# Optimization experiments

Hardware: AMD Instinct MI355X
Metric: run time of the kernel (lower is better)

Reference implementation:

```python
import jax, jax.numpy as jnp
import numpy as np

ALPHA = 2.0  # spikingjelly default ATan surrogate alpha
EPS = 1e-5   # BatchNorm eps

@jax.custom_vjp
def heaviside_atan(x):
    return (x >= 0.0).astype(x.dtype)

def _ha_fwd(x):
    return heaviside_atan(x), x

def _ha_bwd(x, g):
    return (g * ALPHA / (2.0 * (1.0 + (jnp.pi / 2.0 * ALPHA * x) ** 2)),)

heaviside_atan.defvjp(_ha_fwd, _ha_bwd)

def lif(x_seq, tau=2.0, v_th=1.0):
    # MultiStepLIFNode, v_reset=0 (hard reset), detach_reset=True
    def step(v, x):
        v = v + (x - v) / tau
        s = heaviside_atan(v - v_th)
        v = v * (1.0 - jax.lax.stop_gradient(s))
        return v, s
    _, spikes = jax.lax.scan(step, jnp.zeros_like(x_seq[0]), x_seq)
    return spikes

def conv_bn(y, Wt, g, b):
    # 1x1 conv (no bias) + BatchNorm2d in training mode over flattened (T*B, H, W)
    y = jnp.einsum('tbchw,oc->tbohw', y, Wt)
    m = y.mean(axis=(0, 1, 3, 4), keepdims=True)
    v = y.var(axis=(0, 1, 3, 4), keepdims=True)
    C = Wt.shape[0]
    return (y - m) / jnp.sqrt(v + EPS) * g.reshape(1, 1, C, 1, 1) + b.reshape(1, 1, C, 1, 1)

def setup_inputs() -> dict:
    key = jax.random.key(0)
    ks = jax.random.split(key, 5)
    T, B, C, H, W = 4, 64, 384, 14, 14
    x = jax.random.normal(ks[0], (T, B, C, H, W), dtype=jnp.float32)
    Wq = jax.random.normal(ks[1], (C, C), dtype=jnp.float32) * 0.02
    Wk = jax.random.normal(ks[2], (C, C), dtype=jnp.float32) * 0.02
    Wv = jax.random.normal(ks[3], (C, C), dtype=jnp.float32) * 0.02
    Wp = jax.random.normal(ks[4], (C, C), dtype=jnp.float32) * 0.02
    ones = jnp.ones((C,), jnp.float32)
    zeros = jnp.zeros((C,), jnp.float32)
    return {"x": x, "Wq": Wq, "Wk": Wk, "Wv": Wv, "Wp": Wp,
            "gq": ones, "bq": zeros, "gk": ones, "bk": zeros,
            "gv": ones, "bv": zeros, "gp": ones, "bp": zeros}

def reference(x, Wq, Wk, Wv, Wp, gq, bq, gk, bk, gv, bv, gp, bp):
    T, B, C, H, W = x.shape
    nh = 8
    dh = C // nh
    N = H * W

    xs = lif(x)  # pre_lif

    def heads(y):  # [T,B,C,H,W] -> [T,B,h,N,dh]
        y = y.reshape(T, B, C, N).transpose(0, 1, 3, 2)
        return y.reshape(T, B, N, nh, dh).transpose(0, 1, 3, 2, 4)

    q = heads(lif(conv_bn(xs, Wq, gq, bq)))
    k = heads(lif(conv_bn(xs, Wk, gk, bk)))
    v = heads(lif(conv_bn(xs, Wv, gv, bv)))

    attn = jnp.einsum('tbhnd,tbhmd->tbhnm', q, k)      # no softmax
    o = jnp.einsum('tbhnm,tbhmd->tbhnd', attn, v) * 0.125
    o = o.transpose(0, 1, 2, 4, 3).reshape(T, B, C, N).reshape(T, B, C, H, W)
    o = lif(o, v_th=0.5)                                # attn_lif
    return conv_bn(o, Wp, gp, bp)                       # proj (no lif)
```

## Files before the change

### kernel.cpp

```cpp
#include <hip/hip_runtime.h>
#include <hip/hip_bf16.h>
#include <stdint.h>

#define T_  4
#define B_  64
#define C_  384
#define N_  196
#define NH  8
#define DH  48
#define TB_ (T_*B_)
#define R_  (T_*B_*N_)
#define NW  12
#define P_  12544
#define NCHX 86
#define NCHO 66

typedef float f32x2 __attribute__((ext_vector_type(2)));

__global__ __launch_bounds__(256) void transpose_w4(const float* __restrict__ s0,
        const float* __restrict__ s1, const float* __restrict__ s2,
        const float* __restrict__ s3, float* __restrict__ dst){
    __shared__ float tile[64][65];
    int m = blockIdx.z;
    const float* src = (m==0)?s0:(m==1)?s1:(m==2)?s2:s3;
    int o0 = blockIdx.x*64, c0 = blockIdx.y*64;
    int lane = threadIdx.x & 63, w = threadIdx.x >> 6;
    for (int r = w; r < 64; r += 4)
        tile[r][lane] = src[(size_t)(o0+r)*C_ + c0 + lane];
    __syncthreads();
    for (int r = w; r < 64; r += 4)
        dst[(size_t)m*C_*C_ + (size_t)(c0+r)*C_ + o0 + lane] = tile[lane][r];
}

__global__ __launch_bounds__(256) void pre_lif(const float* __restrict__ x,
                                               uint32_t* __restrict__ maskXS,
                                               unsigned long long* __restrict__ maskT){
    int b = blockIdx.x / NW;
    int w = blockIdx.x % NW;
    int n = threadIdx.x;
    if (n >= N_) return;
    int wv = n >> 6, lane = n & 63;
    float v[32];
#pragma unroll
    for (int j=0;j<32;j++) v[j] = 0.f;
#pragma unroll
    for (int t=0;t<T_;t++){
        int tb = t*B_ + b;
        uint32_t word = 0;
#pragma unroll
        for (int j=0;j<32;j++){
            int c = w*32 + j;
            float xv = x[((size_t)tb*C_ + c)*N_ + n];
            v[j] = v[j] + (xv - v[j])*0.5f;
            if (v[j] >= 1.0f){ word |= (1u<<j); v[j] = 0.f; }
        }
        maskXS[((size_t)tb*N_ + n)*NW + w] = word;
        int g = tb*4 + wv, kc = g/12, kw = g - kc*12;
#pragma unroll
        for (int j=0;j<32;j++){
            unsigned long long bal = __ballot((int)((word>>j)&1u));
            if (lane == 0)
                maskT[((size_t)kc*C_ + (w*32+j))*12 + kw] = bal;
        }
    }
}

__global__ __launch_bounds__(256) void gram(const unsigned long long* __restrict__ maskT,
                                            unsigned int* __restrict__ Gu, int nch){
    __shared__ unsigned int tile[64][49];
    int tid = threadIdx.x, wave = tid>>6, lane = tid&63;
    int kg = blockIdx.x, rg = blockIdx.y, cg = blockIdx.z;
    for (int i=tid; i<64*49; i+=256) ((unsigned int*)tile)[i] = 0u;
    __syncthreads();
    int kc = kg*4 + wave;
    if (kc < nch){
        const uint4* rp = (const uint4*)(maskT + ((size_t)kc*C_ + rg*64 + lane)*12);
        uint32_t row[24];
#pragma unroll
        for (int q=0;q<6;q++){
            uint4 a = rp[q];
            row[4*q]=a.x; row[4*q+1]=a.y; row[4*q+2]=a.z; row[4*q+3]=a.w;
        }
        for (int cc=0; cc<48; cc++){
            const uint4* cp = (const uint4*)(maskT + ((size_t)kc*C_ + cg*48 + cc)*12);
            uint32_t col[24];
#pragma unroll
            for (int q=0;q<6;q++){
                uint4 a = cp[q];
                col[4*q]=a.x; col[4*q+1]=a.y; col[4*q+2]=a.z; col[4*q+3]=a.w;
            }
            unsigned int s = 0;
#pragma unroll
            for (int q=0;q<24;q++) s += (unsigned int)__popc(row[q]&col[q]);
            atomicAdd(&tile[lane][cc], s);
        }
    }
    __syncthreads();
    for (int i=tid; i<64*48; i+=256){
        int r = i/48, cc = i%48;
        unsigned int v = tile[r][cc];
        if (v) atomicAdd(&Gu[(size_t)(rg*64+r)*C_ + cg*48 + cc], v);
    }
}

__global__ __launch_bounds__(384) void bn_from_gram(const unsigned int* __restrict__ Gu,
        const float* __restrict__ WTall,
        const float* __restrict__ g0, const float* __restrict__ b0,
        const float* __restrict__ g1, const float* __restrict__ b1,
        const float* __restrict__ g2, const float* __restrict__ b2,
        float* __restrict__ scaleOut, float* __restrict__ shiftOut, int wtBase){
    __shared__ float w4[384][4];
    __shared__ float sred[8][6];
    int t = threadIdx.x, wave = t>>6, lane = t&63;
    int br = blockIdx.y;
    const float* WT = WTall + (size_t)(wtBase+br)*C_*C_;
    int o0 = blockIdx.x*4;
    float4 wv = *(const float4*)(WT + (size_t)t*C_ + o0);
    w4[t][0]=wv.x; w4[t][1]=wv.y; w4[t][2]=wv.z; w4[t][3]=wv.w;
    __syncthreads();
    float h0=0.f,h1=0.f,h2=0.f,h3=0.f;
#pragma unroll 4
    for (int c=0;c<C_;c++){
        float gv = (float)Gu[(size_t)c*C_ + t];
        float4 wc = *(const float4*)&w4[c][0];
        h0 += gv*wc.x; h1 += gv*wc.y; h2 += gv*wc.z; h3 += gv*wc.w;
    }
    float cnt = (float)Gu[(size_t)t*C_ + t];
    float p0=wv.x*h0, p1=wv.y*h1, p2=wv.z*h2, p3=wv.w*h3;
    float q0=cnt*wv.x, q1=cnt*wv.y, q2=cnt*wv.z, q3=cnt*wv.w;
#pragma unroll
    for (int off=32; off>0; off>>=1){
        p0+=__shfl_down(p0,off); p1+=__shfl_down(p1,off);
        p2+=__shfl_down(p2,off); p3+=__shfl_down(p3,off);
        q0+=__shfl_down(q0,off); q1+=__shfl_down(q1,off);
        q2+=__shfl_down(q2,off); q3+=__shfl_down(q3,off);
    }
    if (lane == 0){
        sred[0][wave]=p0; sred[1][wave]=p1; sred[2][wave]=p2; sred[3][wave]=p3;
        sred[4][wave]=q0; sred[5][wave]=q1; sred[6][wave]=q2; sred[7][wave]=q3;
    }
    __syncthreads();
    if (t < 4){
        const float* g  = (br==0)?g0:(br==1)?g1:g2;
        const float* bb = (br==0)?b0:(br==1)?b1:b2;
        float ss = ((sred[t][0]+sred[t][1])+(sred[t][2]+sred[t][3]))+(sred[t][4]+sred[t][5]);
        float sm = ((sred[4+t][0]+sred[4+t][1])+(sred[4+t][2]+sred[4+t][3]))+(sred[4+t][4]+sred[4+t][5]);
        float m   = sm / (float)R_;
        float var = ss / (float)R_ - m*m;
        float sc  = g[o0+t] / sqrtf(var + 1e-5f);
        scaleOut[br*C_ + o0+t] = sc;
        shiftOut[br*C_ + o0+t] = bb[o0+t] - m*sc;
    }
}

__global__ __launch_bounds__(256) void conv_lif3(const uint32_t* __restrict__ mask,
        const float* __restrict__ WTall,
        const float* __restrict__ scaleAll, const float* __restrict__ shiftAll,
        uint32_t* __restrict__ moQ, uint32_t* __restrict__ moK, uint32_t* __restrict__ moV){
    __shared__ uint16_t lst[4][416];
    __shared__ float scLDS[3*C_];
    __shared__ float shLDS[3*C_];
    int tid = threadIdx.x, wave = tid>>6, lane = tid&63;
    int pix0 = blockIdx.x*4 + wave;
    for (int i=tid; i<3*C_; i+=256){ scLDS[i]=scaleAll[i]; shLDS[i]=shiftAll[i]; }
    __syncthreads();

    float v0[6]={0,0,0,0,0,0}, v1[6]={0,0,0,0,0,0}, v2[6]={0,0,0,0,0,0};
    for (int t=0;t<T_;t++){
        size_t pix = (size_t)t*P_ + pix0;
        const uint4* m4 = (const uint4*)(mask + pix*NW);
        uint4 ma = m4[0], mb = m4[1], mc = m4[2];
        uint32_t mwv[12] = {ma.x,ma.y,ma.z,ma.w, mb.x,mb.y,mb.z,mb.w, mc.x,mc.y,mc.z,mc.w};
        int cnt = 0;
#pragma unroll
        for (int w=0;w<12;w++) cnt += __popc(mwv[w]);
        if (lane < 12){
            int off = 0;
            uint32_t mybits = 0;
#pragma unroll
            for (int w=0;w<12;w++){
                if (w < lane) off += __popc(mwv[w]);
                if (w == lane) mybits = mwv[w];
            }
            while (mybits){
                lst[wave][off++] = (uint16_t)((lane<<5) + __builtin_ctz(mybits));
                mybits &= mybits - 1;
            }
        }
        __syncthreads();

#pragma unroll
        for (int br=0; br<3; ++br){
            const float* WT = WTall + (size_t)br*C_*C_ + lane;
            float ya[6]={0,0,0,0,0,0}, yb[6]={0,0,0,0,0,0};
            float yc[6]={0,0,0,0,0,0}, yd[6]={0,0,0,0,0,0};
            int i = 0;
            for (; i+3 < cnt; i += 4){
                ushort4 cs = *(const ushort4*)&lst[wave][i];
                const float* q0 = WT + (size_t)cs.x*C_;
                const float* q1 = WT + (size_t)cs.y*C_;
                const float* q2 = WT + (size_t)cs.z*C_;
                const float* q3 = WT + (size_t)cs.w*C_;
#pragma unroll
                for (int j=0;j<6;j++){
                    ya[j] += q0[j<<6]; yb[j] += q1[j<<6];
                    yc[j] += q2[j<<6]; yd[j] += q3[j<<6];
                }
            }
            for (; i < cnt; ++i){
                int c = lst[wave][i];
                const float* q0 = WT + (size_t)c*C_;
#pragma unroll
                for (int j=0;j<6;j++) ya[j] += q0[j<<6];
            }
            float* vs = (br==0)?v0:(br==1)?v1:v2;
            uint32_t words[12];
#pragma unroll
            for (int j=0;j<6;j++){
                int o = (j<<6) + lane;
                float val = ((ya[j]+yb[j])+(yc[j]+yd[j]))*scLDS[br*C_+o] + shLDS[br*C_+o];
                float vv = vs[j];
                vv = vv + (val - vv)*0.5f;
                int s = (vv >= 1.0f);
                unsigned long long bal = __ballot(s);
                if (s) vv = 0.f;
                vs[j] = vv;
                words[2*j]   = (uint32_t)bal;
                words[2*j+1] = (uint32_t)(bal>>32);
            }
            if (lane == 0){
                uint32_t* mo = (br==0)?moQ:(br==1)?moK:moV;
                uint4* o4 = (uint4*)(mo + pix*NW);
                o4[0] = make_uint4(words[0],words[1],words[2],words[3]);
                o4[1] = make_uint4(words[4],words[5],words[6],words[7]);
                o4[2] = make_uint4(words[8],words[9],words[10],words[11]);
            }
        }
        __syncthreads();
    }
}

__global__ __launch_bounds__(256) void attn_O(const uint32_t* __restrict__ mq,
                                              const uint32_t* __restrict__ mk,
                                              const uint32_t* __restrict__ mv,
                                              uint32_t* __restrict__ aCnt){
    __shared__ unsigned long long kT[DH][4];
    __shared__ unsigned long long vT[DH][4];
    __shared__ uint32_t Cp[DH*25];

    int h  = blockIdx.x & 7;
    int tb = blockIdx.x >> 3;
    int tid = threadIdx.x, wv = tid>>6, lane = tid&63;
    int sw  = (h*DH) >> 5;
    int shf = (h*DH) & 31;

    unsigned long long q = 0, kk = 0, vvv = 0;
    if (tid < N_){
        const uint32_t* pq = mq + ((size_t)tb*N_ + tid)*NW + sw;
        const uint32_t* pk = mk + ((size_t)tb*N_ + tid)*NW + sw;
        const uint32_t* pv = mv + ((size_t)tb*N_ + tid)*NW + sw;
        unsigned long long lo, hi;
        lo = pq[0]; hi = pq[1];
        q   = (shf ? ((lo>>16) | (hi<<16)) : (lo | (hi<<32))) & 0xFFFFFFFFFFFFULL;
        lo = pk[0]; hi = pk[1];
        kk  = (shf ? ((lo>>16) | (hi<<16)) : (lo | (hi<<32))) & 0xFFFFFFFFFFFFULL;
        lo = pv[0]; hi = pv[1];
        vvv = (shf ? ((lo>>16) | (hi<<16)) : (lo | (hi<<32))) & 0xFFFFFFFFFFFFULL;
    }
#pragma unroll 1
    for (int d=0; d<DH; d++){
        unsigned long long bk_ = __ballot((int)((kk >>d)&1ull));
        unsigned long long bv_ = __ballot((int)((vvv>>d)&1ull));
        if (lane == 0){ kT[d][wv] = bk_; vT[d][wv] = bv_; }
    }
    __syncthreads();

    if (tid < 240){
        int j  = tid / 5;
        int dg = tid % 5;
        int d0 = dg*10;
        int d1 = (dg==4) ? 48 : d0+10;
        unsigned long long ka=kT[j][0], kb=kT[j][1], kc=kT[j][2], kd=kT[j][3];
        for (int d=d0; d<d1; d+=2){
            uint32_t c0 = (uint32_t)(__popcll(ka&vT[d][0]) + __popcll(kb&vT[d][1])
                        + __popcll(kc&vT[d][2]) + __popcll(kd&vT[d][3]));
            uint32_t c1 = (uint32_t)(__popcll(ka&vT[d+1][0]) + __popcll(kb&vT[d+1][1])
                        + __popcll(kc&vT[d+1][2]) + __popcll(kd&vT[d+1][3]));
            Cp[j*25 + (d>>1)] = c0 | (c1<<16);
        }
    }
    __syncthreads();

    if (tid < N_){
        uint32_t acc[24];
#pragma unroll
        for (int p=0;p<24;p++) acc[p] = 0u;
        unsigned long long qb = q;
        while (qb){
            int j = __builtin_ctzll(qb); qb &= qb-1;
            const uint32_t* row = &Cp[j*25];
#pragma unroll
            for (int p=0;p<24;p++) acc[p] += row[p];
        }
        uint4* ap = (uint4*)(aCnt + (((size_t)tb*NH + h)*N_ + tid)*24);
        ap[0] = make_uint4(acc[0], acc[1], acc[2], acc[3]);
        ap[1] = make_uint4(acc[4], acc[5], acc[6], acc[7]);
        ap[2] = make_uint4(acc[8], acc[9], acc[10],acc[11]);
        ap[3] = make_uint4(acc[12],acc[13],acc[14],acc[15]);
        ap[4] = make_uint4(acc[16],acc[17],acc[18],acc[19]);
        ap[5] = make_uint4(acc[20],acc[21],acc[22],acc[23]);
    }
}

__global__ __launch_bounds__(64) void attn_lif(const uint32_t* __restrict__ aCnt,
                                               uint16_t* __restrict__ mo,
                                               unsigned long long* __restrict__ maskT){
    int pg  = blockIdx.x;
    int c16 = blockIdx.y;
    int lane = threadIdx.x;
    int pix0 = pg*64 + lane;
    int b = pix0 / N_;
    int n = pix0 - b*N_;
    int h = c16 / 3, sub = c16 - h*3;
    float vm[16];
#pragma unroll
    for (int cc=0;cc<16;cc++) vm[cc] = 0.f;
#pragma unroll
    for (int t=0;t<T_;t++){
        int tb = t*B_ + b;
        const uint4* ap = (const uint4*)(aCnt + (((size_t)tb*NH + h)*N_ + n)*24 + sub*8);
        uint4 A = ap[0], Bv = ap[1];
        uint32_t cw[8] = {A.x,A.y,A.z,A.w, Bv.x,Bv.y,Bv.z,Bv.w};
        uint32_t bits = 0;
#pragma unroll
        for (int cc=0;cc<16;cc++){
            uint32_t a = (cc&1) ? (cw[cc>>1]>>16) : (cw[cc>>1]&0xFFFFu);
            float o = 0.125f*(float)a;
            vm[cc] = vm[cc] + (o - vm[cc])*0.5f;
            if (vm[cc] >= 0.5f){ bits |= (1u<<cc); vm[cc] = 0.f; }
        }
        mo[((size_t)t*P_ + pix0)*24 + c16] = (uint16_t)bits;
        int g = t*196 + pg, kc = g/12, kw = g - kc*12;
#pragma unroll
        for (int cc=0;cc<16;cc++){
            unsigned long long bal = __ballot((int)((bits>>cc)&1u));
            if (lane == 0)
                maskT[((size_t)kc*C_ + c16*16 + cc)*12 + kw] = bal;
        }
    }
}

__global__ __launch_bounds__(256) void proj_out(const uint32_t* __restrict__ mask,
                                                const float* __restrict__ WT,
                                                const float* __restrict__ scale,
                                                const float* __restrict__ shift,
                                                float* __restrict__ out){
    __shared__ float tile[192][49];
    __shared__ uint16_t lst[4][392];
    int bid = blockIdx.x;
    int tb = bid>>3, r7 = bid&7, nq = r7>>1, ch = r7&1;
    int n0 = nq*49, c0 = ch*192;
    int tid = threadIdx.x, wave = tid>>6, lane = tid&63;
    float sc[3], sh[3];
#pragma unroll
    for (int i=0;i<3;i++){
        sc[i] = scale[c0+(i<<6)+lane];
        sh[i] = shift[c0+(i<<6)+lane];
    }
    for (int p=wave; p<49; p+=4){
        size_t pix = (size_t)tb*N_ + n0 + p;
        const uint4* m4 = (const uint4*)(mask + pix*NW);
        uint4 ma = m4[0], mb = m4[1], mc = m4[2];
        uint32_t mwv[12] = {ma.x,ma.y,ma.z,ma.w, mb.x,mb.y,mb.z,mb.w, mc.x,mc.y,mc.z,mc.w};
        int cnt = 0;
#pragma unroll
        for (int w=0;w<12;w++) cnt += __popc(mwv[w]);
        if (lane < 12){
            int off = 0;
            uint32_t mybits = 0;
#pragma unroll
            for (int w=0;w<12;w++){
                if (w < lane) off += __popc(mwv[w]);
                if (w == lane) mybits = mwv[w];
            }
            while (mybits){
                lst[wave][off++] = (uint16_t)((lane<<5) + __builtin_ctz(mybits));
                mybits &= mybits - 1;
            }
        }
        float ya[3]={0,0,0}, yb[3]={0,0,0}, yc[3]={0,0,0}, yd[3]={0,0,0};
        int i = 0;
        for (; i+3 < cnt; i += 4){
            ushort4 cs = *(const ushort4*)&lst[wave][i];
            const float* q0 = WT + (size_t)cs.x*C_ + c0 + lane;
            const float* q1 = WT + (size_t)cs.y*C_ + c0 + lane;
            const float* q2 = WT + (size_t)cs.z*C_ + c0 + lane;
            const float* q3 = WT + (size_t)cs.w*C_ + c0 + lane;
#pragma unroll
            for (int j=0;j<3;j++){
                ya[j] += q0[j<<6]; yb[j] += q1[j<<6];
                yc[j] += q2[j<<6]; yd[j] += q3[j<<6];
            }
        }
        for (; i < cnt; ++i){
            int c = lst[wave][i];
            const float* q0 = WT + (size_t)c*C_ + c0 + lane;
#pragma unroll
            for (int j=0;j<3;j++) ya[j] += q0[j<<6];
        }
#pragma unroll
        for (int j=0;j<3;j++)
            tile[(j<<6)+lane][p] = ((ya[j]+yb[j])+(yc[j]+yd[j]))*sc[j] + sh[j];
    }
    __syncthreads();
    for (int r=wave; r<192; r+=4){
        if (lane < 49)
            out[((size_t)tb*C_ + c0 + r)*N_ + n0 + lane] = tile[r][lane];
    }
}

extern "C" void kernel_launch(void* const* d_in, const int* in_sizes, int n_in,
                              void* d_out, int out_size, void* d_ws, size_t ws_size,
                              hipStream_t stream) {
    const float* x  = (const float*)d_in[0];
    const float* Wq = (const float*)d_in[1];
    const float* Wk = (const float*)d_in[2];
    const float* Wv = (const float*)d_in[3];
    const float* Wp = (const float*)d_in[4];
    const float* gq = (const float*)d_in[5];
    const float* bq = (const float*)d_in[6];
    const float* gk = (const float*)d_in[7];
    const float* bk = (const float*)d_in[8];
    const float* gv = (const float*)d_in[9];
    const float* bv = (const float*)d_in[10];
    const float* gp = (const float*)d_in[11];
    const float* bp = (const float*)d_in[12];

    char* w = (char*)d_ws;
    size_t off = 0;
    uint32_t* maskXS = (uint32_t*)(w + off); off += (size_t)R_*NW*4;
    uint32_t* maskQ  = (uint32_t*)(w + off); off += (size_t)R_*NW*4;
    uint32_t* maskK  = (uint32_t*)(w + off); off += (size_t)R_*NW*4;
    uint32_t* maskV  = (uint32_t*)(w + off); off += (size_t)R_*NW*4;
    float* WTall = (float*)(w + off); off += (size_t)4*C_*C_*4;
    unsigned long long* maskTX = (unsigned long long*)(w + off); off += (size_t)NCHX*C_*12*8;
    unsigned long long* maskTO = (unsigned long long*)(w + off); off += (size_t)NCHO*C_*12*8;
    unsigned int* GuX = (unsigned int*)(w + off); off += (size_t)C_*C_*4;
    unsigned int* GuO = (unsigned int*)(w + off); off += (size_t)C_*C_*4;
    size_t zbytes = (size_t)NCHX*C_*12*8 + (size_t)NCHO*C_*12*8 + 2*(size_t)C_*C_*4;
    uint32_t* aCnt = (uint32_t*)(w + off); off += (size_t)R_*NH*24*4;
    float* scaleB = (float*)(w + off); off += (size_t)4*C_*4;
    float* shiftB = (float*)(w + off); off += (size_t)4*C_*4;
    uint32_t* maskOL = maskXS;

    hipMemsetAsync(maskTX, 0, zbytes, stream);

    transpose_w4<<<dim3(6,6,4),256,0,stream>>>(Wq, Wk, Wv, Wp, WTall);

    pre_lif<<<B_*NW,256,0,stream>>>(x, maskXS, maskTX);

    gram<<<dim3((NCHX+3)/4,6,8),256,0,stream>>>(maskTX, GuX, NCHX);
    bn_from_gram<<<dim3(96,3),384,0,stream>>>(GuX, WTall, gq,bq, gk,bk, gv,bv,
                                              scaleB, shiftB, 0);

    conv_lif3<<<P_/4,256,0,stream>>>(maskXS, WTall, scaleB, shiftB,
                                     maskQ, maskK, maskV);

    attn_O<<<TB_*NH,256,0,stream>>>(maskQ, maskK, maskV, aCnt);
    attn_lif<<<dim3(196,24),64,0,stream>>>(aCnt, (uint16_t*)maskOL, maskTO);

    gram<<<dim3((NCHO+3)/4,6,8),256,0,stream>>>(maskTO, GuO, NCHO);
    bn_from_gram<<<dim3(96,1),384,0,stream>>>(GuO, WTall, gp,bp, gp,bp, gp,bp,
                                              scaleB + 3*C_, shiftB + 3*C_, 3);

    proj_out<<<TB_*8,256,0,stream>>>(maskOL, WTall + (size_t)3*C_*C_,
                                     scaleB + 3*C_, shiftB + 3*C_, (float*)d_out);
}
```

Measured before the change: 376.5 us.

## Fuse memset into weight-transpose kernel, split conv_lif per branch, relayout attention counts

```diff
diff --git a/kernel.cpp b/kernel.cpp
--- a/kernel.cpp
+++ b/kernel.cpp
@@ -14,16 +14,26 @@
 #define P_  12544
 #define NCHX 86
 #define NCHO 66
+#define NZBLK 414
 
 typedef float f32x2 __attribute__((ext_vector_type(2)));
 
-__global__ __launch_bounds__(256) void transpose_w4(const float* __restrict__ s0,
+__global__ __launch_bounds__(256) void prep(const float* __restrict__ s0,
         const float* __restrict__ s1, const float* __restrict__ s2,
-        const float* __restrict__ s3, float* __restrict__ dst){
+        const float* __restrict__ s3, float* __restrict__ dst,
+        uint4* __restrict__ zbase){
+    int blk = blockIdx.x;
+    if (blk >= 144){
+        int z = blk - 144;
+        uint4* p = zbase + (size_t)z*1024 + (size_t)threadIdx.x*4;
+        uint4 zero = make_uint4(0,0,0,0);
+        p[0]=zero; p[1]=zero; p[2]=zero; p[3]=zero;
+        return;
+    }
     __shared__ float tile[64][65];
-    int m = blockIdx.z;
+    int m = blk/36, rem = blk%36;
     const float* src = (m==0)?s0:(m==1)?s1:(m==2)?s2:s3;
-    int o0 = blockIdx.x*64, c0 = blockIdx.y*64;
+    int o0 = (rem/6)*64, c0 = (rem%6)*64;
     int lane = threadIdx.x & 63, w = threadIdx.x >> 6;
     for (int r = w; r < 64; r += 4)
         tile[r][lane] = src[(size_t)(o0+r)*C_ + c0 + lane];
@@ -119,7 +129,7 @@
     w4[t][0]=wv.x; w4[t][1]=wv.y; w4[t][2]=wv.z; w4[t][3]=wv.w;
     __syncthreads();
     float h0=0.f,h1=0.f,h2=0.f,h3=0.f;
-#pragma unroll 4
+#pragma unroll 8
     for (int c=0;c<C_;c++){
         float gv = (float)Gu[(size_t)c*C_ + t];
         float4 wc = *(const float4*)&w4[c][0];
@@ -153,19 +163,19 @@
     }
 }
 
-__global__ __launch_bounds__(256) void conv_lif3(const uint32_t* __restrict__ mask,
-        const float* __restrict__ WTall,
-        const float* __restrict__ scaleAll, const float* __restrict__ shiftAll,
-        uint32_t* __restrict__ moQ, uint32_t* __restrict__ moK, uint32_t* __restrict__ moV){
+__global__ __launch_bounds__(256) void conv_lif_b(const uint32_t* __restrict__ mask,
+        const float* __restrict__ WTbr,
+        const float* __restrict__ scale, const float* __restrict__ shift,
+        uint32_t* __restrict__ mo){
     __shared__ uint16_t lst[4][416];
-    __shared__ float scLDS[3*C_];
-    __shared__ float shLDS[3*C_];
+    __shared__ float scLDS[C_];
+    __shared__ float shLDS[C_];
     int tid = threadIdx.x, wave = tid>>6, lane = tid&63;
     int pix0 = blockIdx.x*4 + wave;
-    for (int i=tid; i<3*C_; i+=256){ scLDS[i]=scaleAll[i]; shLDS[i]=shiftAll[i]; }
-    __syncthreads();
-
-    float v0[6]={0,0,0,0,0,0}, v1[6]={0,0,0,0,0,0}, v2[6]={0,0,0,0,0,0};
+    for (int i=tid; i<C_; i+=256){ scLDS[i]=scale[i]; shLDS[i]=shift[i]; }
+    __syncthreads();
+
+    float vs[6]={0,0,0,0,0,0};
     for (int t=0;t<T_;t++){
         size_t pix = (size_t)t*P_ + pix0;
         const uint4* m4 = (const uint4*)(mask + pix*NW);
@@ -189,52 +199,47 @@
         }
         __syncthreads();
 
-#pragma unroll
-        for (int br=0; br<3; ++br){
-            const float* WT = WTall + (size_t)br*C_*C_ + lane;
-            float ya[6]={0,0,0,0,0,0}, yb[6]={0,0,0,0,0,0};
-            float yc[6]={0,0,0,0,0,0}, yd[6]={0,0,0,0,0,0};
-            int i = 0;
-            for (; i+3 < cnt; i += 4){
-                ushort4 cs = *(const ushort4*)&lst[wave][i];
-                const float* q0 = WT + (size_t)cs.x*C_;
-                const float* q1 = WT + (size_t)cs.y*C_;
-                const float* q2 = WT + (size_t)cs.z*C_;
-                const float* q3 = WT + (size_t)cs.w*C_;
-#pragma unroll
-                for (int j=0;j<6;j++){
-                    ya[j] += q0[j<<6]; yb[j] += q1[j<<6];
-                    yc[j] += q2[j<<6]; yd[j] += q3[j<<6];
-                }
-            }
-            for (; i < cnt; ++i){
-                int c = lst[wave][i];
-                const float* q0 = WT + (size_t)c*C_;
-#pragma unroll
-                for (int j=0;j<6;j++) ya[j] += q0[j<<6];
-            }
-            float* vs = (br==0)?v0:(br==1)?v1:v2;
-            uint32_t words[12];
+        const float* WT = WTbr + lane;
+        float ya[6]={0,0,0,0,0,0}, yb[6]={0,0,0,0,0,0};
+        float yc[6]={0,0,0,0,0,0}, yd[6]={0,0,0,0,0,0};
+        int i = 0;
+        for (; i+3 < cnt; i += 4){
+            ushort4 cs = *(const ushort4*)&lst[wave][i];
+            const float* q0 = WT + (size_t)cs.x*C_;
+            const float* q1 = WT + (size_t)cs.y*C_;
+            const float* q2 = WT + (size_t)cs.z*C_;
+            const float* q3 = WT + (size_t)cs.w*C_;
 #pragma unroll
             for (int j=0;j<6;j++){
-                int o = (j<<6) + lane;
-                float val = ((ya[j]+yb[j])+(yc[j]+yd[j]))*scLDS[br*C_+o] + shLDS[br*C_+o];
-                float vv = vs[j];
-                vv = vv + (val - vv)*0.5f;
-                int s = (vv >= 1.0f);
-                unsigned long long bal = __ballot(s);
-                if (s) vv = 0.f;
-                vs[j] = vv;
-                words[2*j]   = (uint32_t)bal;
-                words[2*j+1] = (uint32_t)(bal>>32);
-            }
-            if (lane == 0){
-                uint32_t* mo = (br==0)?moQ:(br==1)?moK:moV;
-                uint4* o4 = (uint4*)(mo + pix*NW);
-                o4[0] = make_uint4(words[0],words[1],words[2],words[3]);
-                o4[1] = make_uint4(words[4],words[5],words[6],words[7]);
-                o4[2] = make_uint4(words[8],words[9],words[10],words[11]);
-            }
+                ya[j] += q0[j<<6]; yb[j] += q1[j<<6];
+                yc[j] += q2[j<<6]; yd[j] += q3[j<<6];
+            }
+        }
+        for (; i < cnt; ++i){
+            int c = lst[wave][i];
+            const float* q0 = WT + (size_t)c*C_;
+#pragma unroll
+            for (int j=0;j<6;j++) ya[j] += q0[j<<6];
+        }
+        uint32_t words[12];
+#pragma unroll
+        for (int j=0;j<6;j++){
+            int o = (j<<6) + lane;
+            float val = ((ya[j]+yb[j])+(yc[j]+yd[j]))*scLDS[o] + shLDS[o];
+            float vv = vs[j];
+            vv = vv + (val - vv)*0.5f;
+            int s = (vv >= 1.0f);
+            unsigned long long bal = __ballot(s);
+            if (s) vv = 0.f;
+            vs[j] = vv;
+            words[2*j]   = (uint32_t)bal;
+            words[2*j+1] = (uint32_t)(bal>>32);
+        }
+        if (lane == 0){
+            uint4* o4 = (uint4*)(mo + pix*NW);
+            o4[0] = make_uint4(words[0],words[1],words[2],words[3]);
+            o4[1] = make_uint4(words[4],words[5],words[6],words[7]);
+            o4[2] = make_uint4(words[8],words[9],words[10],words[11]);
         }
         __syncthreads();
     }
@@ -302,13 +307,13 @@
 #pragma unroll
             for (int p=0;p<24;p++) acc[p] += row[p];
         }
-        uint4* ap = (uint4*)(aCnt + (((size_t)tb*NH + h)*N_ + tid)*24);
-        ap[0] = make_uint4(acc[0], acc[1], acc[2], acc[3]);
-        ap[1] = make_uint4(acc[4], acc[5], acc[6], acc[7]);
-        ap[2] = make_uint4(acc[8], acc[9], acc[10],acc[11]);
-        ap[3] = make_uint4(acc[12],acc[13],acc[14],acc[15]);
-        ap[4] = make_uint4(acc[16],acc[17],acc[18],acc[19]);
-        ap[5] = make_uint4(acc[20],acc[21],acc[22],acc[23]);
+        size_t hb = ((size_t)tb*NH + h)*3;
+#pragma unroll
+        for (int sub=0; sub<3; ++sub){
+            uint4* ap = (uint4*)(aCnt + ((hb + sub)*N_ + tid)*8);
+            ap[0] = make_uint4(acc[sub*8+0], acc[sub*8+1], acc[sub*8+2], acc[sub*8+3]);
+            ap[1] = make_uint4(acc[sub*8+4], acc[sub*8+5], acc[sub*8+6], acc[sub*8+7]);
+        }
     }
 }
 
@@ -328,7 +333,7 @@
 #pragma unroll
     for (int t=0;t<T_;t++){
         int tb = t*B_ + b;
-        const uint4* ap = (const uint4*)(aCnt + (((size_t)tb*NH + h)*N_ + n)*24 + sub*8);
+        const uint4* ap = (const uint4*)(aCnt + ((((size_t)tb*NH + h)*3 + sub)*N_ + n)*8);
         uint4 A = ap[0], Bv = ap[1];
         uint32_t cw[8] = {A.x,A.y,A.z,A.w, Bv.x,Bv.y,Bv.z,Bv.w};
         uint32_t bits = 0;
@@ -447,15 +452,12 @@
     unsigned long long* maskTO = (unsigned long long*)(w + off); off += (size_t)NCHO*C_*12*8;
     unsigned int* GuX = (unsigned int*)(w + off); off += (size_t)C_*C_*4;
     unsigned int* GuO = (unsigned int*)(w + off); off += (size_t)C_*C_*4;
-    size_t zbytes = (size_t)NCHX*C_*12*8 + (size_t)NCHO*C_*12*8 + 2*(size_t)C_*C_*4;
     uint32_t* aCnt = (uint32_t*)(w + off); off += (size_t)R_*NH*24*4;
     float* scaleB = (float*)(w + off); off += (size_t)4*C_*4;
     float* shiftB = (float*)(w + off); off += (size_t)4*C_*4;
     uint32_t* maskOL = maskXS;
 
-    hipMemsetAsync(maskTX, 0, zbytes, stream);
-
-    transpose_w4<<<dim3(6,6,4),256,0,stream>>>(Wq, Wk, Wv, Wp, WTall);
+    prep<<<144+NZBLK,256,0,stream>>>(Wq, Wk, Wv, Wp, WTall, (uint4*)maskTX);
 
     pre_lif<<<B_*NW,256,0,stream>>>(x, maskXS, maskTX);
 
@@ -463,8 +465,10 @@
     bn_from_gram<<<dim3(96,3),384,0,stream>>>(GuX, WTall, gq,bq, gk,bk, gv,bv,
                                               scaleB, shiftB, 0);
 
-    conv_lif3<<<P_/4,256,0,stream>>>(maskXS, WTall, scaleB, shiftB,
-                                     maskQ, maskK, maskV);
+    uint32_t* Ms[3] = {maskQ, maskK, maskV};
+    for (int br=0; br<3; ++br)
+        conv_lif_b<<<P_/4,256,0,stream>>>(maskXS, WTall + (size_t)br*C_*C_,
+                                          scaleB + br*C_, shiftB + br*C_, Ms[br]);
 
     attn_O<<<TB_*NH,256,0,stream>>>(maskQ, maskK, maskV, aCnt);
     attn_lif<<<dim3(196,24),64,0,stream>>>(aCnt, (uint16_t*)maskOL, maskTO);
```

Result: faster. 360.4 us (-4.3%).
